# Optimization experiments

Measured on AMD Instinct MI355X. Metric: run time of the kernel, lower is better.

The kernel has to match this reference:

```python
import jax, jax.numpy as jnp
import numpy as np

HEAD_DIM = 128
Q_HEADS = 24
KV_HEADS = 8
TARGET_KV_HEADS = 32
HIDDEN = 3072


def setup_inputs() -> dict:
    key = jax.random.key(0)
    ks = jax.random.split(key, 8)
    bsz, q_len = 4, 2048
    return {
        "hidden_states": jax.random.normal(ks[0], (bsz, q_len, HIDDEN), jnp.float32),
        "rope_rotary_cos_sin": jax.random.normal(ks[1], (bsz, q_len, HEAD_DIM), jnp.float32),
        "context_lengths": jax.random.randint(ks[2], (bsz,), 0, q_len, jnp.int32),
        "kvcache_start_index": jax.random.randint(ks[3], (bsz,), 0, q_len, jnp.int32),
        "kv_cache": jax.random.normal(ks[4], (bsz, 2, KV_HEADS, 4096, HEAD_DIM), jnp.float32),
        "Wq": jax.random.normal(ks[5], (Q_HEADS * HEAD_DIM, HIDDEN), jnp.float32) * 0.02,
        "Wk": jax.random.normal(ks[6], (KV_HEADS * HEAD_DIM, HIDDEN), jnp.float32) * 0.02,
        "Wv": jax.random.normal(ks[7], (KV_HEADS * HEAD_DIM, HIDDEN), jnp.float32) * 0.02,
        "Wo": jax.random.normal(jax.random.fold_in(key, 99), (HIDDEN, Q_HEADS * HEAD_DIM), jnp.float32) * 0.02,
    }


def reference(hidden_states, rope_rotary_cos_sin, context_lengths, kvcache_start_index,
              kv_cache, Wq, Wk, Wv, Wo):
    bsz, q_len, _ = hidden_states.shape
    # QKV projections (nn.Linear, no bias): y = x @ W^T
    q = jnp.einsum('bsh,dh->bsd', hidden_states, Wq)
    k = jnp.einsum('bsh,dh->bsd', hidden_states, Wk)
    v = jnp.einsum('bsh,dh->bsd', hidden_states, Wv)
    # [b, heads, s, d]
    q = q.reshape(bsz, q_len, Q_HEADS, HEAD_DIM).transpose(0, 2, 1, 3)
    k = k.reshape(bsz, q_len, KV_HEADS, HEAD_DIM).transpose(0, 2, 1, 3)
    v = v.reshape(bsz, q_len, KV_HEADS, HEAD_DIM).transpose(0, 2, 1, 3)
    # GQA head padding: each kv head repeated `repeats` times contiguously
    repeats = TARGET_KV_HEADS // KV_HEADS
    k = jnp.repeat(k, repeats, axis=1)
    v = jnp.repeat(v, repeats, axis=1)
    qk_scale = jnp.asarray(HEAD_DIM ** -0.5, dtype=hidden_states.dtype)
    q = q * qk_scale
    # trt::fake_attention is a placeholder: returns (query.clone(), kv_cache.clone()).
    # Faithful to the source math: attn_output = scaled query; kv_cache passes through.
    attn_output = q  # [b, Q_HEADS, s, d]
    attn_output = attn_output.transpose(0, 2, 1, 3).reshape(bsz, q_len, Q_HEADS * HEAD_DIM)
    # current (3072) == o_proj.in_features (3072): no repeat/truncate branch taken
    out = jnp.einsum('bsd,od->bso', attn_output, Wo)
    return (out, kv_cache)
```

## Files before the change

kernel.cpp:

```cpp
#include <hip/hip_runtime.h>


typedef __attribute__((ext_vector_type(8))) __bf16 bf16x8;
typedef __attribute__((ext_vector_type(4))) float f32x4;

__device__ __forceinline__ unsigned short f2bf(float f) {
  union { float f; unsigned u; } v; v.f = f;
  unsigned r = v.u + 0x7fffu + ((v.u >> 16) & 1u);
  return (unsigned short)(r >> 16);
}

__global__ void cast_f32_to_bf16(const float4* __restrict__ in,
                                 ushort4* __restrict__ out, int n4) {
  int i = blockIdx.x * blockDim.x + threadIdx.x;
  int stride = gridDim.x * blockDim.x;
  for (; i < n4; i += stride) {
    float4 v = in[i];
    ushort4 o;
    o.x = f2bf(v.x); o.y = f2bf(v.y); o.z = f2bf(v.z); o.w = f2bf(v.w);
    out[i] = o;
  }
}

__global__ void transpose_cast(const float* __restrict__ in,
                               ushort* __restrict__ out, int R, int C) {
  __shared__ float tile[32][33];
  const int tc = blockIdx.x * 32;
  const int tr = blockIdx.y * 32;
  const int lx = threadIdx.x & 31;
  const int ly = threadIdx.x >> 5;
#pragma unroll
  for (int i = 0; i < 32; i += 8)
    tile[ly + i][lx] = in[(size_t)(tr + ly + i) * C + (tc + lx)];
  __syncthreads();
#pragma unroll
  for (int i = 0; i < 32; i += 8)
    out[(size_t)(tc + ly + i) * R + (tr + lx)] = f2bf(tile[lx][ly + i]);
}

typedef const __attribute__((address_space(1))) void* gptr_t;
typedef __attribute__((address_space(3))) void* lptr_t;

__device__ __forceinline__ void gload16(const void* g, void* l) {
  __builtin_amdgcn_global_load_lds((gptr_t)g, (lptr_t)l, 16, 0, 0);
}

#define BAR   do { asm volatile("" ::: "memory"); __builtin_amdgcn_s_barrier(); asm volatile("" ::: "memory"); } while (0)
#define LGKM0 asm volatile("s_waitcnt lgkmcnt(0)" ::: "memory")
#define VM(n) asm volatile("s_waitcnt vmcnt(" #n ")" ::: "memory")

__global__ __launch_bounds__(512, 2)
void gemm_big(const ushort* __restrict__ A, const ushort* __restrict__ B,
              float* __restrict__ C, int M, int N, int K) {
  __shared__ __align__(16) char smem[114688];

  const int t    = threadIdx.x;
  const int w    = t >> 6;
  const int lane = t & 63;
  const int wr   = w >> 2;
  const int wc   = w & 3;
  const int fr   = lane & 15;
  const int g    = lane >> 4;

  const int nwg = gridDim.x;
  const int cpx = nwg >> 3;
  const int wg  = (blockIdx.x & 7) * cpx + (blockIdx.x >> 3);
  const int nbx = N / 192;
  const int bx  = wg % nbx, by = wg / nbx;
  const int rowBase = by * 256, colBase = bx * 192;

  const int sr   = lane >> 3;
  const int scol = ((lane & 7) ^ sr) << 3;
  const ushort* Ag = A + (size_t)(rowBase + w * 8 + sr) * K + scol;
  const ushort* Bg = B + (size_t)(colBase + w * 8 + sr) * K + scol;
  const int wofs = w * 1024;

#define STAGE_A_LOW(kt)  do { char* d_ = smem + ((kt) & 1) * 57344 + wofs;          \
    const ushort* s_ = Ag + (size_t)(kt) * 64;                                      \
    gload16(s_, d_); gload16(s_ + (size_t)64 * K, d_ + 8192); } while (0)
#define STAGE_A_HIGH(kt) do { char* d_ = smem + ((kt) & 1) * 57344 + 16384 + wofs;  \
    const ushort* s_ = Ag + (size_t)128 * K + (size_t)(kt) * 64;                    \
    gload16(s_, d_); gload16(s_ + (size_t)64 * K, d_ + 8192); } while (0)
#define STAGE_B(kt)      do { char* d_ = smem + ((kt) & 1) * 57344 + 32768 + wofs;  \
    const ushort* s_ = Bg + (size_t)(kt) * 64;                                      \
    gload16(s_, d_); gload16(s_ + (size_t)64 * K, d_ + 8192);                       \
    gload16(s_ + (size_t)128 * K, d_ + 16384); } while (0)

  const int aBase = (wr * 128 + fr) * 128;
  const int bBase = 32768 + (wc * 48 + fr) * 128;
  const int cs0   = (g ^ (fr & 7)) << 4;
  const int cs1   = ((4 | g) ^ (fr & 7)) << 4;

#define READ_A(dst, bo, MH, CS) do {                                  \
    const char* p_ = smem + (bo) + aBase + (MH) * 8192 + (CS);        \
    dst[0] = *(const bf16x8*)(p_);                                    \
    dst[1] = *(const bf16x8*)(p_ + 2048);                             \
    dst[2] = *(const bf16x8*)(p_ + 4096);                             \
    dst[3] = *(const bf16x8*)(p_ + 6144); } while (0)
#define READ_B(dst, bo, CS) do {                                      \
    const char* p_ = smem + (bo) + bBase + (CS);                      \
    dst[0] = *(const bf16x8*)(p_);                                    \
    dst[1] = *(const bf16x8*)(p_ + 2048);                             \
    dst[2] = *(const bf16x8*)(p_ + 4096); } while (0)
#define MFMA_Q(MH, aset, bset) do {                                   \
    _Pragma("unroll") for (int mi_ = 0; mi_ < 4; ++mi_)               \
    _Pragma("unroll") for (int ni_ = 0; ni_ < 3; ++ni_)               \
      acc[(MH) * 4 + mi_][ni_] = __builtin_amdgcn_mfma_f32_16x16x32_bf16( \
          aset[mi_], bset[ni_], acc[(MH) * 4 + mi_][ni_], 0, 0, 0); } while (0)

  f32x4 acc[8][3];
#pragma unroll
  for (int m = 0; m < 8; ++m)
#pragma unroll
    for (int n = 0; n < 3; ++n)
      acc[m][n] = f32x4{0.f, 0.f, 0.f, 0.f};

  bf16x8 aA[4], aB[4], Bk0[3], Bk1[3];

  const int nt = K >> 6;

  STAGE_A_LOW(0); STAGE_B(0); STAGE_A_HIGH(0);
  STAGE_A_LOW(1); STAGE_B(1); STAGE_A_HIGH(1);
  VM(7);
  BAR;
  READ_A(aA, 0, 0, cs0);
  READ_B(Bk0, 0, cs0);

  for (int T = 0; T < nt; ++T) {
    const int bo  = (T & 1) * 57344;
    const int bon = 57344 - bo;
    const bool stg = (T + 2) < nt;
    READ_A(aB, bo, 0, cs1);
    READ_B(Bk1, bo, cs1);
    BAR; LGKM0;
    __builtin_amdgcn_s_setprio(1); MFMA_Q(0, aA, Bk0); __builtin_amdgcn_s_setprio(0);
    BAR;
    READ_A(aA, bo, 1, cs0);
    BAR; LGKM0;
    __builtin_amdgcn_s_setprio(1); MFMA_Q(0, aB, Bk1); __builtin_amdgcn_s_setprio(0);
    BAR;
    if (stg) STAGE_B(T + 2);
    READ_A(aB, bo, 1, cs1);
    BAR; LGKM0;
    __builtin_amdgcn_s_setprio(1); MFMA_Q(1, aA, Bk0); __builtin_amdgcn_s_setprio(0);
    if (T < nt - 2) { VM(3); } else { VM(0); }
    BAR;
    if (stg) { STAGE_A_LOW(T + 2); STAGE_A_HIGH(T + 2); }
    if (T + 1 < nt) { READ_A(aA, bon, 0, cs0); READ_B(Bk0, bon, cs0); }
    BAR; LGKM0;
    __builtin_amdgcn_s_setprio(1); MFMA_Q(1, aB, Bk1); __builtin_amdgcn_s_setprio(0);
    BAR;
  }

#undef STAGE_A_LOW
#undef STAGE_A_HIGH
#undef STAGE_B
#undef READ_A
#undef READ_B
#undef MFMA_Q

  const int orow = rowBase + wr * 128 + (g << 2);
  const int ocol = colBase + wc * 48 + fr;
#pragma unroll
  for (int mi = 0; mi < 8; ++mi)
#pragma unroll
    for (int ni = 0; ni < 3; ++ni)
#pragma unroll
      for (int i = 0; i < 4; ++i)
        C[(size_t)(orow + mi * 16 + i) * N + (ocol + ni * 16)] = acc[mi][ni][i];
}

template <int OUT_BF16>
__global__ void gemm_bt(const ushort* __restrict__ A, const ushort* __restrict__ B,
                        void* __restrict__ Cv, int M, int N, int K, float scale) {
  __shared__ __align__(16) ushort As[128 * 32];
  __shared__ __align__(16) ushort Bs[128 * 32];

  const int t    = threadIdx.x;
  const int w    = t >> 6;
  const int lane = t & 63;
  const int wr   = w >> 1, wc = w & 1;
  const int fr   = lane & 15;
  const int g    = lane >> 4;

  const int nwg  = gridDim.x;
  const int cpx  = nwg >> 3;
  const int wg   = (blockIdx.x & 7) * cpx + (blockIdx.x >> 3);
  const int nbx  = N >> 7;
  const int bx   = wg % nbx;
  const int by   = wg / nbx;
  const int rowBase = by * 128;
  const int colBase = bx * 128;

  const int r0 = t >> 2;
  const int sc = ((t & 3) ^ ((t >> 3) & 3)) << 3;
  const ushort* Ag0 = A + (size_t)(rowBase + r0) * K + sc;
  const ushort* Ag1 = A + (size_t)(rowBase + 64 + r0) * K + sc;
  const ushort* Bg0 = B + (size_t)(colBase + r0) * K + sc;
  const ushort* Bg1 = B + (size_t)(colBase + 64 + r0) * K + sc;
  ushort* Al0 = &As[w * 512];
  ushort* Al1 = &As[2048 + w * 512];
  ushort* Bl0 = &Bs[w * 512];
  ushort* Bl1 = &Bs[2048 + w * 512];

  const int swz8 = (g ^ ((fr >> 1) & 3)) << 3;

  f32x4 acc[4][4];
#pragma unroll
  for (int m = 0; m < 4; ++m)
#pragma unroll
    for (int n = 0; n < 4; ++n)
      acc[m][n] = f32x4{0.f, 0.f, 0.f, 0.f};

  for (int k0 = 0; k0 < K; k0 += 32) {
    __syncthreads();
    gload16(Ag0 + k0, Al0);
    gload16(Ag1 + k0, Al1);
    gload16(Bg0 + k0, Bl0);
    gload16(Bg1 + k0, Bl1);
    __syncthreads();

    bf16x8 a[4], b[4];
#pragma unroll
    for (int m = 0; m < 4; ++m)
      a[m] = *(const bf16x8*)&As[(wr * 64 + m * 16 + fr) * 32 + swz8];
#pragma unroll
    for (int n = 0; n < 4; ++n)
      b[n] = *(const bf16x8*)&Bs[(wc * 64 + n * 16 + fr) * 32 + swz8];

#pragma unroll
    for (int m = 0; m < 4; ++m)
#pragma unroll
      for (int n = 0; n < 4; ++n)
        acc[m][n] = __builtin_amdgcn_mfma_f32_16x16x32_bf16(a[m], b[n], acc[m][n], 0, 0, 0);
  }

  const int orow = rowBase + wr * 64 + (g << 2);
  const int ocol = colBase + wc * 64 + fr;
#pragma unroll
  for (int m = 0; m < 4; ++m)
#pragma unroll
    for (int n = 0; n < 4; ++n)
#pragma unroll
      for (int i = 0; i < 4; ++i) {
        const size_t idx = (size_t)(orow + m * 16 + i) * N + (ocol + n * 16);
        float v = acc[m][n][i] * scale;
        if (OUT_BF16) ((ushort*)Cv)[idx] = f2bf(v);
        else          ((float*)Cv)[idx]  = v;
      }
}

extern "C" void kernel_launch(void* const* d_in, const int* in_sizes, int n_in,
                              void* d_out, int out_size, void* d_ws, size_t ws_size,
                              hipStream_t stream) {
  const float* hs = (const float*)d_in[0];
  const float* kv = (const float*)d_in[4];
  const float* Wq = (const float*)d_in[5];
  const float* Wo = (const float*)d_in[8];

  const int M = 8192, H = 3072;
  const int OUT_ELEMS = M * H;

  float* out = (float*)d_out;

  ushort* Xb   = (ushort*)d_ws;
  ushort* Wob  = Xb + (size_t)M * H;
  ushort* WqTb = Wob + (size_t)H * H;
  ushort* Wb   = (ushort*)(out + OUT_ELEMS);

  cast_f32_to_bf16<<<2048, 256, 0, stream>>>((const float4*)hs, (ushort4*)Xb, (M * H) / 4);
  cast_f32_to_bf16<<<1024, 256, 0, stream>>>((const float4*)Wo, (ushort4*)Wob, (H * H) / 4);
  transpose_cast<<<dim3(H / 32, H / 32), 256, 0, stream>>>(Wq, WqTb, H, H);

  const float qk_scale = 0.08838834764831845f;
  gemm_bt<1><<<(H / 128) * (H / 128), 256, 0, stream>>>(Wob, WqTb, (void*)Wb, H, H, H, qk_scale);
  gemm_big<<<(M / 256) * (H / 192), 512, 0, stream>>>(Xb, Wb, out, M, H, H);

  hipMemcpyAsync(out + OUT_ELEMS, kv, (size_t)in_sizes[4] * sizeof(float),
                 hipMemcpyDeviceToDevice, stream);
}
```

Measured before the change: 328.4 us.

## Use tuned big GEMM for weight-product and fuse kv_cache copy into GEMM epilogue

The small 128x128 gemm_bt kernel used to form the fused Wo·Wq weight product is replaced by the pipelined 256x192 gemm kernel, now templated to emit scaled bf16 output. The separate hipMemcpyAsync of kv_cache is folded into the tail of the main GEMM, with each block copying its own chunk once its output is written. The bf16 weight product moves into workspace when the workspace is large enough, so the copy no longer overwrites it. This removes a slow GEMM and a separate copy launch, but the copy now runs in the GEMM tail and relies on the chunk size dividing evenly across the 512 blocks.

```diff
diff --git a/kernel.cpp b/kernel.cpp
--- a/kernel.cpp
+++ b/kernel.cpp
@@ -49,9 +49,12 @@
 #define LGKM0 asm volatile("s_waitcnt lgkmcnt(0)" ::: "memory")
 #define VM(n) asm volatile("s_waitcnt vmcnt(" #n ")" ::: "memory")
 
+template <int OUT_BF16>
 __global__ __launch_bounds__(512, 2)
-void gemm_big(const ushort* __restrict__ A, const ushort* __restrict__ B,
-              float* __restrict__ C, int M, int N, int K) {
+void gemm5(const ushort* __restrict__ A, const ushort* __restrict__ B,
+           void* __restrict__ Cv, int M, int N, int K, float scale,
+           const float4* __restrict__ kvsrc, float4* __restrict__ kvdst,
+           int kvchunk) {
   __shared__ __align__(16) char smem[114688];
 
   const int t    = threadIdx.x;
@@ -166,88 +169,18 @@
 #pragma unroll
     for (int ni = 0; ni < 3; ++ni)
 #pragma unroll
-      for (int i = 0; i < 4; ++i)
-        C[(size_t)(orow + mi * 16 + i) * N + (ocol + ni * 16)] = acc[mi][ni][i];
-}
-
-template <int OUT_BF16>
-__global__ void gemm_bt(const ushort* __restrict__ A, const ushort* __restrict__ B,
-                        void* __restrict__ Cv, int M, int N, int K, float scale) {
-  __shared__ __align__(16) ushort As[128 * 32];
-  __shared__ __align__(16) ushort Bs[128 * 32];
-
-  const int t    = threadIdx.x;
-  const int w    = t >> 6;
-  const int lane = t & 63;
-  const int wr   = w >> 1, wc = w & 1;
-  const int fr   = lane & 15;
-  const int g    = lane >> 4;
-
-  const int nwg  = gridDim.x;
-  const int cpx  = nwg >> 3;
-  const int wg   = (blockIdx.x & 7) * cpx + (blockIdx.x >> 3);
-  const int nbx  = N >> 7;
-  const int bx   = wg % nbx;
-  const int by   = wg / nbx;
-  const int rowBase = by * 128;
-  const int colBase = bx * 128;
-
-  const int r0 = t >> 2;
-  const int sc = ((t & 3) ^ ((t >> 3) & 3)) << 3;
-  const ushort* Ag0 = A + (size_t)(rowBase + r0) * K + sc;
-  const ushort* Ag1 = A + (size_t)(rowBase + 64 + r0) * K + sc;
-  const ushort* Bg0 = B + (size_t)(colBase + r0) * K + sc;
-  const ushort* Bg1 = B + (size_t)(colBase + 64 + r0) * K + sc;
-  ushort* Al0 = &As[w * 512];
-  ushort* Al1 = &As[2048 + w * 512];
-  ushort* Bl0 = &Bs[w * 512];
-  ushort* Bl1 = &Bs[2048 + w * 512];
-
-  const int swz8 = (g ^ ((fr >> 1) & 3)) << 3;
-
-  f32x4 acc[4][4];
-#pragma unroll
-  for (int m = 0; m < 4; ++m)
-#pragma unroll
-    for (int n = 0; n < 4; ++n)
-      acc[m][n] = f32x4{0.f, 0.f, 0.f, 0.f};
-
-  for (int k0 = 0; k0 < K; k0 += 32) {
-    __syncthreads();
-    gload16(Ag0 + k0, Al0);
-    gload16(Ag1 + k0, Al1);
-    gload16(Bg0 + k0, Bl0);
-    gload16(Bg1 + k0, Bl1);
-    __syncthreads();
-
-    bf16x8 a[4], b[4];
-#pragma unroll
-    for (int m = 0; m < 4; ++m)
-      a[m] = *(const bf16x8*)&As[(wr * 64 + m * 16 + fr) * 32 + swz8];
-#pragma unroll
-    for (int n = 0; n < 4; ++n)
-      b[n] = *(const bf16x8*)&Bs[(wc * 64 + n * 16 + fr) * 32 + swz8];
-
-#pragma unroll
-    for (int m = 0; m < 4; ++m)
-#pragma unroll
-      for (int n = 0; n < 4; ++n)
-        acc[m][n] = __builtin_amdgcn_mfma_f32_16x16x32_bf16(a[m], b[n], acc[m][n], 0, 0, 0);
-  }
-
-  const int orow = rowBase + wr * 64 + (g << 2);
-  const int ocol = colBase + wc * 64 + fr;
-#pragma unroll
-  for (int m = 0; m < 4; ++m)
-#pragma unroll
-    for (int n = 0; n < 4; ++n)
-#pragma unroll
       for (int i = 0; i < 4; ++i) {
-        const size_t idx = (size_t)(orow + m * 16 + i) * N + (ocol + n * 16);
-        float v = acc[m][n][i] * scale;
+        const size_t idx = (size_t)(orow + mi * 16 + i) * N + (ocol + ni * 16);
+        float v = acc[mi][ni][i] * scale;
         if (OUT_BF16) ((ushort*)Cv)[idx] = f2bf(v);
         else          ((float*)Cv)[idx]  = v;
       }
+
+  if (kvdst) {
+    size_t beg = (size_t)blockIdx.x * kvchunk;
+    for (int i = t; i < kvchunk; i += 512)
+      kvdst[beg + i] = kvsrc[beg + i];
+  }
 }
 
 extern "C" void kernel_launch(void* const* d_in, const int* in_sizes, int n_in,
@@ -260,22 +193,35 @@
 
   const int M = 8192, H = 3072;
   const int OUT_ELEMS = M * H;
+  const int nkv  = in_sizes[4];
+  const int nkv4 = nkv / 4;
+  const int kvchunk = nkv4 / 512;
 
   float* out = (float*)d_out;
 
   ushort* Xb   = (ushort*)d_ws;
   ushort* Wob  = Xb + (size_t)M * H;
   ushort* WqTb = Wob + (size_t)H * H;
-  ushort* Wb   = (ushort*)(out + OUT_ELEMS);
+  const size_t WS_NEED = 2ull * ((size_t)M * H + 3ull * (size_t)H * H);
+  const bool ws_ok = ws_size >= WS_NEED;
+  ushort* Wb = ws_ok ? (WqTb + (size_t)H * H) : (ushort*)(out + OUT_ELEMS);
 
   cast_f32_to_bf16<<<2048, 256, 0, stream>>>((const float4*)hs, (ushort4*)Xb, (M * H) / 4);
   cast_f32_to_bf16<<<1024, 256, 0, stream>>>((const float4*)Wo, (ushort4*)Wob, (H * H) / 4);
   transpose_cast<<<dim3(H / 32, H / 32), 256, 0, stream>>>(Wq, WqTb, H, H);
 
   const float qk_scale = 0.08838834764831845f;
-  gemm_bt<1><<<(H / 128) * (H / 128), 256, 0, stream>>>(Wob, WqTb, (void*)Wb, H, H, H, qk_scale);
-  gemm_big<<<(M / 256) * (H / 192), 512, 0, stream>>>(Xb, Wb, out, M, H, H);
-
-  hipMemcpyAsync(out + OUT_ELEMS, kv, (size_t)in_sizes[4] * sizeof(float),
-                 hipMemcpyDeviceToDevice, stream);
-}
+
+  gemm5<1><<<(H / 256) * (H / 192), 512, 0, stream>>>(
+      Wob, WqTb, (void*)Wb, H, H, H, qk_scale, nullptr, nullptr, 0);
+
+  const float4* kvs = ws_ok ? (const float4*)kv : nullptr;
+  float4* kvd = ws_ok ? (float4*)(out + OUT_ELEMS) : nullptr;
+  gemm5<0><<<(M / 256) * (H / 192), 512, 0, stream>>>(
+      Xb, Wb, (void*)out, M, H, H, 1.0f, kvs, kvd, kvchunk);
+
+  if (!ws_ok) {
+    hipMemcpyAsync(out + OUT_ELEMS, kv, (size_t)nkv * sizeof(float),
+                   hipMemcpyDeviceToDevice, stream);
+  }
+}
```

Result: no change. 333.7 us (+1.6%).

## Merge prep kernels and overlap hidden-state cast and KV copy with weight GEMM

Applied to the files above, without the earlier changes.

The two weight-prep kernels (Wq transpose-cast and Wo cast) become one launch. The hidden-state cast and the KV-cache copy are folded into the same grid as the Wo·WqT weight GEMM, using 192 dedicated blocks, so this memory-bound work runs alongside the compute-bound GEMM. The fused weight is written to workspace when it is large enough, which frees the kv output region so the copy can run concurrently. This removes launches and serialization but adds a workspace-size dependency, and the copy blocks compete with the GEMM for bandwidth and CUs.

```diff
diff --git a/kernel.cpp b/kernel.cpp
--- a/kernel.cpp
+++ b/kernel.cpp
@@ -10,32 +10,10 @@
   return (unsigned short)(r >> 16);
 }
 
-__global__ void cast_f32_to_bf16(const float4* __restrict__ in,
-                                 ushort4* __restrict__ out, int n4) {
-  int i = blockIdx.x * blockDim.x + threadIdx.x;
-  int stride = gridDim.x * blockDim.x;
-  for (; i < n4; i += stride) {
-    float4 v = in[i];
-    ushort4 o;
-    o.x = f2bf(v.x); o.y = f2bf(v.y); o.z = f2bf(v.z); o.w = f2bf(v.w);
-    out[i] = o;
-  }
-}
-
-__global__ void transpose_cast(const float* __restrict__ in,
-                               ushort* __restrict__ out, int R, int C) {
-  __shared__ float tile[32][33];
-  const int tc = blockIdx.x * 32;
-  const int tr = blockIdx.y * 32;
-  const int lx = threadIdx.x & 31;
-  const int ly = threadIdx.x >> 5;
-#pragma unroll
-  for (int i = 0; i < 32; i += 8)
-    tile[ly + i][lx] = in[(size_t)(tr + ly + i) * C + (tc + lx)];
-  __syncthreads();
-#pragma unroll
-  for (int i = 0; i < 32; i += 8)
-    out[(size_t)(tc + ly + i) * R + (tr + lx)] = f2bf(tile[lx][ly + i]);
+__device__ __forceinline__ ushort4 cast4(float4 v) {
+  ushort4 o;
+  o.x = f2bf(v.x); o.y = f2bf(v.y); o.z = f2bf(v.z); o.w = f2bf(v.w);
+  return o;
 }
 
 typedef const __attribute__((address_space(1))) void* gptr_t;
@@ -49,9 +27,128 @@
 #define LGKM0 asm volatile("s_waitcnt lgkmcnt(0)" ::: "memory")
 #define VM(n) asm volatile("s_waitcnt vmcnt(" #n ")" ::: "memory")
 
+__global__ void prep(const float* __restrict__ Wq, ushort* __restrict__ WqT,
+                     const float4* __restrict__ Wo4, ushort4* __restrict__ Wob4) {
+  __shared__ float tile[32][33];
+  const int H = 3072;
+  if (blockIdx.x < 9216) {
+    const int id = blockIdx.x;
+    const int tc = (id % 96) * 32;
+    const int tr = (id / 96) * 32;
+    const int lx = threadIdx.x & 31;
+    const int ly = threadIdx.x >> 5;
+#pragma unroll
+    for (int i = 0; i < 32; i += 8)
+      tile[ly + i][lx] = Wq[(size_t)(tr + ly + i) * H + (tc + lx)];
+    __syncthreads();
+#pragma unroll
+    for (int i = 0; i < 32; i += 8)
+      WqT[(size_t)(tc + ly + i) * H + (tr + lx)] = f2bf(tile[lx][ly + i]);
+  } else {
+    const int n4 = (H * H) / 4;
+    int i = (blockIdx.x - 9216) * 256 + threadIdx.x;
+    for (; i < n4; i += 1024 * 256)
+      Wob4[i] = cast4(Wo4[i]);
+  }
+}
+
+__global__ __launch_bounds__(256)
+void mega(const ushort* __restrict__ A,
+          const ushort* __restrict__ B,
+          ushort* __restrict__ Cw,
+          const float4* __restrict__ hs4, ushort4* __restrict__ Xb4,
+          const float4* __restrict__ kvsrc, float4* __restrict__ kvdst,
+          float scale) {
+  __shared__ __align__(16) ushort As[128 * 32];
+  __shared__ __align__(16) ushort Bs[128 * 32];
+
+  const int HH = 3072;
+  if (blockIdx.x < 192) {
+    const int gtid = blockIdx.x * 256 + threadIdx.x;
+    const int gstr = 192 * 256;
+    const int nx4 = (8192 * HH) / 4;
+    for (int i = gtid; i < nx4; i += gstr)
+      Xb4[i] = cast4(hs4[i]);
+    if (kvdst) {
+      const int nkv4 = 8388608;
+      for (int i = gtid; i < nkv4; i += gstr)
+        kvdst[i] = kvsrc[i];
+    }
+    return;
+  }
+
+  const int bid  = blockIdx.x - 192;
+  const int t    = threadIdx.x;
+  const int w    = t >> 6;
+  const int lane = t & 63;
+  const int wr   = w >> 1, wc = w & 1;
+  const int fr   = lane & 15;
+  const int g    = lane >> 4;
+
+  const int wg  = (bid & 7) * 72 + (bid >> 3);
+  const int nbx = HH >> 7;
+  const int bx  = wg % nbx, by = wg / nbx;
+  const int rowBase = by * 128, colBase = bx * 128;
+
+  const int r0 = t >> 2;
+  const int sc = ((t & 3) ^ ((t >> 3) & 3)) << 3;
+  const ushort* Ag0 = A + (size_t)(rowBase + r0) * HH + sc;
+  const ushort* Ag1 = A + (size_t)(rowBase + 64 + r0) * HH + sc;
+  const ushort* Bg0 = B + (size_t)(colBase + r0) * HH + sc;
+  const ushort* Bg1 = B + (size_t)(colBase + 64 + r0) * HH + sc;
+  ushort* Al0 = &As[w * 512];
+  ushort* Al1 = &As[2048 + w * 512];
+  ushort* Bl0 = &Bs[w * 512];
+  ushort* Bl1 = &Bs[2048 + w * 512];
+
+  const int swz8 = (g ^ ((fr >> 1) & 3)) << 3;
+
+  f32x4 acc[4][4];
+#pragma unroll
+  for (int m = 0; m < 4; ++m)
+#pragma unroll
+    for (int n = 0; n < 4; ++n)
+      acc[m][n] = f32x4{0.f, 0.f, 0.f, 0.f};
+
+  for (int k0 = 0; k0 < HH; k0 += 32) {
+    __syncthreads();
+    gload16(Ag0 + k0, Al0);
+    gload16(Ag1 + k0, Al1);
+    gload16(Bg0 + k0, Bl0);
+    gload16(Bg1 + k0, Bl1);
+    __syncthreads();
+
+    bf16x8 a[4], b[4];
+#pragma unroll
+    for (int m = 0; m < 4; ++m)
+      a[m] = *(const bf16x8*)&As[(wr * 64 + m * 16 + fr) * 32 + swz8];
+#pragma unroll
+    for (int n = 0; n < 4; ++n)
+      b[n] = *(const bf16x8*)&Bs[(wc * 64 + n * 16 + fr) * 32 + swz8];
+
+#pragma unroll
+    for (int m = 0; m < 4; ++m)
+#pragma unroll
+      for (int n = 0; n < 4; ++n)
+        acc[m][n] = __builtin_amdgcn_mfma_f32_16x16x32_bf16(a[m], b[n], acc[m][n], 0, 0, 0);
+  }
+
+  const int orow = rowBase + wr * 64 + (g << 2);
+  const int ocol = colBase + wc * 64 + fr;
+#pragma unroll
+  for (int m = 0; m < 4; ++m)
+#pragma unroll
+    for (int n = 0; n < 4; ++n)
+#pragma unroll
+      for (int i = 0; i < 4; ++i) {
+        const size_t idx = (size_t)(orow + m * 16 + i) * HH + (ocol + n * 16);
+        Cw[idx] = f2bf(acc[m][n][i] * scale);
+      }
+}
+
 __global__ __launch_bounds__(512, 2)
-void gemm_big(const ushort* __restrict__ A, const ushort* __restrict__ B,
-              float* __restrict__ C, int M, int N, int K) {
+void gemm5(const ushort* __restrict__ A, const ushort* __restrict__ B,
+           float* __restrict__ C, int M, int N, int K) {
   __shared__ __align__(16) char smem[114688];
 
   const int t    = threadIdx.x;
@@ -170,86 +267,6 @@
         C[(size_t)(orow + mi * 16 + i) * N + (ocol + ni * 16)] = acc[mi][ni][i];
 }
 
-template <int OUT_BF16>
-__global__ void gemm_bt(const ushort* __restrict__ A, const ushort* __restrict__ B,
-                        void* __restrict__ Cv, int M, int N, int K, float scale) {
-  __shared__ __align__(16) ushort As[128 * 32];
-  __shared__ __align__(16) ushort Bs[128 * 32];
-
-  const int t    = threadIdx.x;
-  const int w    = t >> 6;
-  const int lane = t & 63;
-  const int wr   = w >> 1, wc = w & 1;
-  const int fr   = lane & 15;
-  const int g    = lane >> 4;
-
-  const int nwg  = gridDim.x;
-  const int cpx  = nwg >> 3;
-  const int wg   = (blockIdx.x & 7) * cpx + (blockIdx.x >> 3);
-  const int nbx  = N >> 7;
-  const int bx   = wg % nbx;
-  const int by   = wg / nbx;
-  const int rowBase = by * 128;
-  const int colBase = bx * 128;
-
-  const int r0 = t >> 2;
-  const int sc = ((t & 3) ^ ((t >> 3) & 3)) << 3;
-  const ushort* Ag0 = A + (size_t)(rowBase + r0) * K + sc;
-  const ushort* Ag1 = A + (size_t)(rowBase + 64 + r0) * K + sc;
-  const ushort* Bg0 = B + (size_t)(colBase + r0) * K + sc;
-  const ushort* Bg1 = B + (size_t)(colBase + 64 + r0) * K + sc;
-  ushort* Al0 = &As[w * 512];
-  ushort* Al1 = &As[2048 + w * 512];
-  ushort* Bl0 = &Bs[w * 512];
-  ushort* Bl1 = &Bs[2048 + w * 512];
-
-  const int swz8 = (g ^ ((fr >> 1) & 3)) << 3;
-
-  f32x4 acc[4][4];
-#pragma unroll
-  for (int m = 0; m < 4; ++m)
-#pragma unroll
-    for (int n = 0; n < 4; ++n)
-      acc[m][n] = f32x4{0.f, 0.f, 0.f, 0.f};
-
-  for (int k0 = 0; k0 < K; k0 += 32) {
-    __syncthreads();
-    gload16(Ag0 + k0, Al0);
-    gload16(Ag1 + k0, Al1);
-    gload16(Bg0 + k0, Bl0);
-    gload16(Bg1 + k0, Bl1);
-    __syncthreads();
-
-    bf16x8 a[4], b[4];
-#pragma unroll
-    for (int m = 0; m < 4; ++m)
-      a[m] = *(const bf16x8*)&As[(wr * 64 + m * 16 + fr) * 32 + swz8];
-#pragma unroll
-    for (int n = 0; n < 4; ++n)
-      b[n] = *(const bf16x8*)&Bs[(wc * 64 + n * 16 + fr) * 32 + swz8];
-
-#pragma unroll
-    for (int m = 0; m < 4; ++m)
-#pragma unroll
-      for (int n = 0; n < 4; ++n)
-        acc[m][n] = __builtin_amdgcn_mfma_f32_16x16x32_bf16(a[m], b[n], acc[m][n], 0, 0, 0);
-  }
-
-  const int orow = rowBase + wr * 64 + (g << 2);
-  const int ocol = colBase + wc * 64 + fr;
-#pragma unroll
-  for (int m = 0; m < 4; ++m)
-#pragma unroll
-    for (int n = 0; n < 4; ++n)
-#pragma unroll
-      for (int i = 0; i < 4; ++i) {
-        const size_t idx = (size_t)(orow + m * 16 + i) * N + (ocol + n * 16);
-        float v = acc[m][n][i] * scale;
-        if (OUT_BF16) ((ushort*)Cv)[idx] = f2bf(v);
-        else          ((float*)Cv)[idx]  = v;
-      }
-}
-
 extern "C" void kernel_launch(void* const* d_in, const int* in_sizes, int n_in,
                               void* d_out, int out_size, void* d_ws, size_t ws_size,
                               hipStream_t stream) {
@@ -260,22 +277,30 @@
 
   const int M = 8192, H = 3072;
   const int OUT_ELEMS = M * H;
+  const int nkv = in_sizes[4];
 
   float* out = (float*)d_out;
 
   ushort* Xb   = (ushort*)d_ws;
   ushort* Wob  = Xb + (size_t)M * H;
   ushort* WqTb = Wob + (size_t)H * H;
-  ushort* Wb   = (ushort*)(out + OUT_ELEMS);
-
-  cast_f32_to_bf16<<<2048, 256, 0, stream>>>((const float4*)hs, (ushort4*)Xb, (M * H) / 4);
-  cast_f32_to_bf16<<<1024, 256, 0, stream>>>((const float4*)Wo, (ushort4*)Wob, (H * H) / 4);
-  transpose_cast<<<dim3(H / 32, H / 32), 256, 0, stream>>>(Wq, WqTb, H, H);
+  const size_t WS_NEED = 2ull * ((size_t)M * H + 3ull * (size_t)H * H);
+  const bool ws_ok = ws_size >= WS_NEED;
+  ushort* Wb = ws_ok ? (WqTb + (size_t)H * H) : (ushort*)(out + OUT_ELEMS);
 
   const float qk_scale = 0.08838834764831845f;
-  gemm_bt<1><<<(H / 128) * (H / 128), 256, 0, stream>>>(Wob, WqTb, (void*)Wb, H, H, H, qk_scale);
-  gemm_big<<<(M / 256) * (H / 192), 512, 0, stream>>>(Xb, Wb, out, M, H, H);
-
-  hipMemcpyAsync(out + OUT_ELEMS, kv, (size_t)in_sizes[4] * sizeof(float),
-                 hipMemcpyDeviceToDevice, stream);
-}
+
+  prep<<<10240, 256, 0, stream>>>(Wq, WqTb, (const float4*)Wo, (ushort4*)Wob);
+
+  const float4* kvs = ws_ok ? (const float4*)kv : nullptr;
+  float4* kvd = ws_ok ? (float4*)(out + OUT_ELEMS) : nullptr;
+  mega<<<768, 256, 0, stream>>>(Wob, WqTb, Wb, (const float4*)hs,
+                                (ushort4*)Xb, kvs, kvd, qk_scale);
+
+  gemm5<<<(M / 256) * (H / 192), 512, 0, stream>>>(Xb, Wb, out, M, H, H);
+
+  if (!ws_ok) {
+    hipMemcpyAsync(out + OUT_ELEMS, kv, (size_t)nkv * sizeof(float),
+                   hipMemcpyDeviceToDevice, stream);
+  }
+}
```

Measured after the change: 375.9 us. +14.5%, slower.
